# Optimization experiments

Measured on AMD Instinct MI355X. Metric: run time of the kernel, lower is better.

Reference implementation:

```python
import jax, jax.numpy as jnp
import numpy as np

B, L, C, H = 1024, 64, 1024, 16  # windows*batch, window area, dim, heads
D = C // H  # head_dim = 64
WIN = 64  # window_size[0]; window_size = (64, 1)


def _relative_position_index():
    coords = np.arange(WIN)
    idx = coords[:, None] - coords[None, :] + (WIN - 1)
    return jnp.asarray(idx, dtype=jnp.int32)  # [L, L]


def setup_inputs() -> dict:
    key = jax.random.key(0)
    ks = jax.random.split(key, 8)
    s = 0.02
    return {
        "hidden_states": jax.random.normal(ks[0], (B, L, C), dtype=jnp.float32),
        "Wq": jax.random.normal(ks[1], (C, C), dtype=jnp.float32) * s,
        "bq": jax.random.normal(ks[2], (C,), dtype=jnp.float32) * s,
        "Wk": jax.random.normal(ks[3], (C, C), dtype=jnp.float32) * s,
        "bk": jax.random.normal(ks[4], (C,), dtype=jnp.float32) * s,
        "Wv": jax.random.normal(ks[5], (C, C), dtype=jnp.float32) * s,
        "bv": jax.random.normal(ks[6], (C,), dtype=jnp.float32) * s,
        "bias_table": jax.random.normal(ks[7], (2 * WIN - 1, H), dtype=jnp.float32) * s,
        "rel_index": _relative_position_index(),
    }


def reference(hidden_states, Wq, bq, Wk, bk, Wv, bv, bias_table, rel_index):
    b, l, c = hidden_states.shape
    # QKV projections -> [b, H, l, D]
    q = (hidden_states @ Wq + bq).reshape(b, l, H, D).transpose(0, 2, 1, 3)
    k = (hidden_states @ Wk + bk).reshape(b, l, H, D).transpose(0, 2, 1, 3)
    v = (hidden_states @ Wv + bv).reshape(b, l, H, D).transpose(0, 2, 1, 3)
    scores = jnp.einsum("bhqd,bhkd->bhqk", q, k) / jnp.sqrt(jnp.float32(D))
    # relative position bias: gather [L, L, H] -> [1, H, L, L]
    rel_bias = bias_table[rel_index]  # [L, L, H]
    scores = scores + rel_bias.transpose(2, 0, 1)[None]
    probs = jax.nn.softmax(scores, axis=-1)  # dropout p=0.0 (eval)
    context = jnp.einsum("bhqk,bhkd->bhqd", probs, v)
    context = context.transpose(0, 2, 1, 3).reshape(b, l, c)
    return context
```

## Files before the change

kernel.cpp:

```cpp
#include <hip/hip_runtime.h>
#include <hip/hip_fp16.h>
#include <stdint.h>

typedef _Float16 f16;
typedef _Float16 f16x8 __attribute__((ext_vector_type(8)));
typedef float f32x4 __attribute__((ext_vector_type(4)));

__device__ __forceinline__ void gload_lds16(const void* g, void* l) {
    __builtin_amdgcn_global_load_lds(
        (const __attribute__((address_space(1))) void*)g,
        (__attribute__((address_space(3))) void*)l,
        16, 0, 0);
}

__global__ __launch_bounds__(256) void convert_x(const float* __restrict__ X,
                                                 f16* __restrict__ Xh) {
    size_t i = ((size_t)blockIdx.x * 256 + threadIdx.x) * 8;
    float4 a = *(const float4*)(X + i);
    float4 b = *(const float4*)(X + i + 4);
    f16x8 o;
    o[0] = (f16)a.x; o[1] = (f16)a.y; o[2] = (f16)a.z; o[3] = (f16)a.w;
    o[4] = (f16)b.x; o[5] = (f16)b.y; o[6] = (f16)b.z; o[7] = (f16)b.w;
    *(f16x8*)(Xh + i) = o;
}

__global__ __launch_bounds__(1024) void transpose_w(const float* __restrict__ Wq,
                                                    const float* __restrict__ Wk,
                                                    const float* __restrict__ Wv,
                                                    f16* __restrict__ Wt) {
    __shared__ float tile[32][33];
    const int w = blockIdx.z;
    const float* W = (w == 0) ? Wq : ((w == 1) ? Wk : Wv);
    const int n0 = blockIdx.x * 32, k0 = blockIdx.y * 32;
    const int tx = threadIdx.x, ty = threadIdx.y;
    tile[ty][tx] = W[(size_t)(k0 + ty) * 1024 + n0 + tx];
    __syncthreads();
    Wt[(size_t)(w * 1024 + n0 + ty) * 1024 + k0 + tx] = (f16)tile[tx][ty];
}

__global__ __launch_bounds__(256) void qkv_gemm(const f16* __restrict__ A,
                                                const f16* __restrict__ Bt,
                                                const float* __restrict__ bq,
                                                const float* __restrict__ bk,
                                                const float* __restrict__ bv,
                                                f16* __restrict__ Out) {
    __shared__ __align__(16) f16 sA[128][32];
    __shared__ __align__(16) f16 sB[128][32];

    const int tid  = threadIdx.x;
    const int wave = tid >> 6, lane = tid & 63;
    const int quad = lane >> 4, l16 = lane & 15;
    const int m0 = blockIdx.y * 128, n0 = blockIdx.x * 128;
    const int wm = (wave & 1) * 64, wn = (wave >> 1) * 64;

    const int srow = lane >> 2;
    const int scol = (lane & 3) * 8;
    const f16* gA = A  + (size_t)(m0 + wave * 32 + srow) * 1024 + scol;
    const f16* gB = Bt + (size_t)(n0 + wave * 32 + srow) * 1024 + scol;
    f16* lA = &sA[wave * 32][0];
    f16* lB = &sB[wave * 32][0];

    f32x4 acc[4][4] = {};

    for (int k0 = 0; k0 < 1024; k0 += 32) {
        gload_lds16(gA + k0,             lA);
        gload_lds16(gA + k0 + 16 * 1024, lA + 16 * 32);
        gload_lds16(gB + k0,             lB);
        gload_lds16(gB + k0 + 16 * 1024, lB + 16 * 32);
        __syncthreads();

        f16x8 af[4], bf[4];
#pragma unroll
        for (int t = 0; t < 4; ++t)
            af[t] = *(const f16x8*)&sA[wm + t * 16 + l16][quad * 8];
#pragma unroll
        for (int t = 0; t < 4; ++t)
            bf[t] = *(const f16x8*)&sB[wn + t * 16 + l16][quad * 8];

#pragma unroll
        for (int mt = 0; mt < 4; ++mt)
#pragma unroll
            for (int nt = 0; nt < 4; ++nt)
                acc[mt][nt] = __builtin_amdgcn_mfma_f32_16x16x32_f16(
                    af[mt], bf[nt], acc[mt][nt], 0, 0, 0);
        __syncthreads();
    }

    const int w_idx = n0 >> 10;
    const float* bias = (w_idx == 0) ? bq : ((w_idx == 1) ? bk : bv);
    f16* out = Out + (size_t)w_idx * (65536UL * 1024UL);
#pragma unroll
    for (int mt = 0; mt < 4; ++mt) {
#pragma unroll
        for (int r = 0; r < 4; ++r) {
            const int m = m0 + wm + mt * 16 + quad * 4 + r;
            const int b = m >> 6, l = m & 63;
#pragma unroll
            for (int nt = 0; nt < 4; ++nt) {
                const int n  = n0 + wn + nt * 16 + l16;
                const int nc = n & 1023;
                const int h = nc >> 6, d = nc & 63;
                const float v = acc[mt][nt][r] + bias[nc];
                out[(((size_t)b * 16 + h) * 64 + l) * 64 + d] = (f16)v;
            }
        }
    }
}

__global__ __launch_bounds__(256) void attn(const f16* __restrict__ QKV,
                                            const float* __restrict__ bias_table,
                                            float* __restrict__ outp) {
    __shared__ __align__(16) f16 sQ[64][72];
    __shared__ __align__(16) f16 sK[64][72];
    __shared__ __align__(16) f16 sVt[64][72];
    __shared__ float sS[64][66];
    __shared__ float sR[64];

    const int bh = blockIdx.x;
    const int h  = bh & 15;
    const int tid  = threadIdx.x;
    const int wave = tid >> 6, lane = tid & 63;
    const int quad = lane >> 4, l16 = lane & 15;

    const f16* Qg = QKV + (size_t)bh * 4096;
    const f16* Kg = Qg + 65536UL * 1024UL;
    const f16* Vg = Kg + 65536UL * 1024UL;

#pragma unroll
    for (int j = 0; j < 2; ++j) {
        const int idx = tid + j * 256;
        const int e = idx * 8;
        const int l = e >> 6, d = e & 63;
        *(f16x8*)&sQ[l][d] = *(const f16x8*)(Qg + e);
        *(f16x8*)&sK[l][d] = *(const f16x8*)(Kg + e);
        f16x8 v = *(const f16x8*)(Vg + e);
#pragma unroll
        for (int i = 0; i < 8; ++i) sVt[d + i][l] = v[i];
    }
    __syncthreads();

    {
        f32x4 acc[4] = {};
#pragma unroll
        for (int k0 = 0; k0 < 64; k0 += 32) {
            f16x8 a = *(const f16x8*)&sQ[wave * 16 + l16][k0 + quad * 8];
#pragma unroll
            for (int nt = 0; nt < 4; ++nt) {
                f16x8 b = *(const f16x8*)&sK[nt * 16 + l16][k0 + quad * 8];
                acc[nt] = __builtin_amdgcn_mfma_f32_16x16x32_f16(a, b, acc[nt], 0, 0, 0);
            }
        }
#pragma unroll
        for (int nt = 0; nt < 4; ++nt) {
            const int jcol = nt * 16 + l16;
#pragma unroll
            for (int r = 0; r < 4; ++r) {
                const int i = wave * 16 + quad * 4 + r;
                const float bias = bias_table[(i - jcol + 63) * 16 + h];
                sS[i][jcol] = acc[nt][r] * 0.125f + bias;
            }
        }
    }
    __syncthreads();

    if (tid < 64) {
        float mx = -1e30f;
#pragma unroll
        for (int j = 0; j < 64; ++j) mx = fmaxf(mx, sS[tid][j]);
        float sum = 0.f;
#pragma unroll
        for (int j = 0; j < 64; ++j) {
            const float e = __expf(sS[tid][j] - mx);
            sum += e;
            sQ[tid][j] = (f16)e;
        }
        sR[tid] = 1.0f / sum;
    }
    __syncthreads();

    {
        f32x4 acc[4] = {};
#pragma unroll
        for (int k0 = 0; k0 < 64; k0 += 32) {
            f16x8 a = *(const f16x8*)&sQ[wave * 16 + l16][k0 + quad * 8];
#pragma unroll
            for (int nt = 0; nt < 4; ++nt) {
                f16x8 b = *(const f16x8*)&sVt[nt * 16 + l16][k0 + quad * 8];
                acc[nt] = __builtin_amdgcn_mfma_f32_16x16x32_f16(a, b, acc[nt], 0, 0, 0);
            }
        }
        const int b = bh >> 4;
#pragma unroll
        for (int nt = 0; nt < 4; ++nt) {
            const int d = nt * 16 + l16;
#pragma unroll
            for (int r = 0; r < 4; ++r) {
                const int i = wave * 16 + quad * 4 + r;
                outp[((size_t)b * 64 + i) * 1024 + h * 64 + d] = acc[nt][r] * sR[i];
            }
        }
    }
}

extern "C" void kernel_launch(void* const* d_in, const int* in_sizes, int n_in,
                              void* d_out, int out_size, void* d_ws, size_t ws_size,
                              hipStream_t stream) {
    const float* X          = (const float*)d_in[0];
    const float* Wq         = (const float*)d_in[1];
    const float* bq         = (const float*)d_in[2];
    const float* Wk         = (const float*)d_in[3];
    const float* bk         = (const float*)d_in[4];
    const float* Wv         = (const float*)d_in[5];
    const float* bv         = (const float*)d_in[6];
    const float* bias_table = (const float*)d_in[7];
    float* out = (float*)d_out;

    f16* Xh  = (f16*)d_ws;
    f16* Wt  = Xh + 67108864UL;
    f16* QKV = Wt + 3145728UL;

    convert_x<<<32768, 256, 0, stream>>>(X, Xh);
    transpose_w<<<dim3(32, 32, 3), dim3(32, 32), 0, stream>>>(Wq, Wk, Wv, Wt);
    qkv_gemm<<<dim3(24, 512), 256, 0, stream>>>(Xh, Wt, bq, bk, bv, QKV);
    attn<<<16384, 256, 0, stream>>>(QKV, bias_table, out);
}
```

Measured before the change: 1.125 ms.

## Swizzle GEMM LDS, store V transposed, and keep attention softmax in registers

The QKV GEMM now XOR-swizzles the LDS column layout to cut bank conflicts on the fragment reads. Its epilogue writes V directly in [b,h,d,l] layout with vectorized f16x4 stores, so attention can load V^T with plain vector copies instead of scattered transposes. Attention keeps scores in MFMA accumulators and does the softmax with cross-lane shuffles. It also caches the per-head bias row in LDS, removing the fp32 score buffer and two block barriers. The trade-off is that correctness now relies on each wave writing and reading only its own rows of sQ, guarded by a waitcnt rather than a barrier.

```diff
diff --git a/kernel.cpp b/kernel.cpp
--- a/kernel.cpp
+++ b/kernel.cpp
@@ -3,6 +3,7 @@
 #include <stdint.h>
 
 typedef _Float16 f16;
+typedef _Float16 f16x4 __attribute__((ext_vector_type(4)));
 typedef _Float16 f16x8 __attribute__((ext_vector_type(8)));
 typedef float f32x4 __attribute__((ext_vector_type(4)));
 
@@ -54,11 +55,13 @@
     const int wm = (wave & 1) * 64, wn = (wave >> 1) * 64;
 
     const int srow = lane >> 2;
-    const int scol = (lane & 3) * 8;
+    const int scol = (((lane & 3) ^ ((lane >> 3) & 3))) * 8;
     const f16* gA = A  + (size_t)(m0 + wave * 32 + srow) * 1024 + scol;
     const f16* gB = Bt + (size_t)(n0 + wave * 32 + srow) * 1024 + scol;
     f16* lA = &sA[wave * 32][0];
     f16* lB = &sB[wave * 32][0];
+
+    const int fcol = (quad ^ ((l16 >> 1) & 3)) * 8;
 
     f32x4 acc[4][4] = {};
 
@@ -72,10 +75,10 @@
         f16x8 af[4], bf[4];
 #pragma unroll
         for (int t = 0; t < 4; ++t)
-            af[t] = *(const f16x8*)&sA[wm + t * 16 + l16][quad * 8];
+            af[t] = *(const f16x8*)&sA[wm + t * 16 + l16][fcol];
 #pragma unroll
         for (int t = 0; t < 4; ++t)
-            bf[t] = *(const f16x8*)&sB[wn + t * 16 + l16][quad * 8];
+            bf[t] = *(const f16x8*)&sB[wn + t * 16 + l16][fcol];
 
 #pragma unroll
         for (int mt = 0; mt < 4; ++mt)
@@ -89,19 +92,38 @@
     const int w_idx = n0 >> 10;
     const float* bias = (w_idx == 0) ? bq : ((w_idx == 1) ? bk : bv);
     f16* out = Out + (size_t)w_idx * (65536UL * 1024UL);
-#pragma unroll
-    for (int mt = 0; mt < 4; ++mt) {
-#pragma unroll
-        for (int r = 0; r < 4; ++r) {
-            const int m = m0 + wm + mt * 16 + quad * 4 + r;
-            const int b = m >> 6, l = m & 63;
+    if (w_idx < 2) {
+#pragma unroll
+        for (int mt = 0; mt < 4; ++mt) {
+#pragma unroll
+            for (int r = 0; r < 4; ++r) {
+                const int m = m0 + wm + mt * 16 + quad * 4 + r;
+                const int b = m >> 6, l = m & 63;
+#pragma unroll
+                for (int nt = 0; nt < 4; ++nt) {
+                    const int n  = n0 + wn + nt * 16 + l16;
+                    const int nc = n & 1023;
+                    const int h = nc >> 6, d = nc & 63;
+                    const float v = acc[mt][nt][r] + bias[nc];
+                    out[(((size_t)b * 16 + h) * 64 + l) * 64 + d] = (f16)v;
+                }
+            }
+        }
+    } else {
+#pragma unroll
+        for (int mt = 0; mt < 4; ++mt) {
+            const int mb = m0 + wm + mt * 16 + quad * 4;
+            const int b = mb >> 6, l = mb & 63;
 #pragma unroll
             for (int nt = 0; nt < 4; ++nt) {
                 const int n  = n0 + wn + nt * 16 + l16;
                 const int nc = n & 1023;
                 const int h = nc >> 6, d = nc & 63;
-                const float v = acc[mt][nt][r] + bias[nc];
-                out[(((size_t)b * 16 + h) * 64 + l) * 64 + d] = (f16)v;
+                f16x4 pv;
+#pragma unroll
+                for (int r = 0; r < 4; ++r)
+                    pv[r] = (f16)(acc[mt][nt][r] + bias[nc]);
+                *(f16x4*)&out[(((size_t)b * 16 + h) * 64 + d) * 64 + l] = pv;
             }
         }
     }
@@ -113,8 +135,7 @@
     __shared__ __align__(16) f16 sQ[64][72];
     __shared__ __align__(16) f16 sK[64][72];
     __shared__ __align__(16) f16 sVt[64][72];
-    __shared__ float sS[64][66];
-    __shared__ float sR[64];
+    __shared__ float sBias[128];
 
     const int bh = blockIdx.x;
     const int h  = bh & 15;
@@ -128,77 +149,76 @@
 
 #pragma unroll
     for (int j = 0; j < 2; ++j) {
-        const int idx = tid + j * 256;
-        const int e = idx * 8;
-        const int l = e >> 6, d = e & 63;
-        *(f16x8*)&sQ[l][d] = *(const f16x8*)(Qg + e);
-        *(f16x8*)&sK[l][d] = *(const f16x8*)(Kg + e);
-        f16x8 v = *(const f16x8*)(Vg + e);
-#pragma unroll
-        for (int i = 0; i < 8; ++i) sVt[d + i][l] = v[i];
-    }
+        const int e = (tid + j * 256) * 8;
+        const int r = e >> 6, c = e & 63;
+        *(f16x8*)&sQ[r][c]  = *(const f16x8*)(Qg + e);
+        *(f16x8*)&sK[r][c]  = *(const f16x8*)(Kg + e);
+        *(f16x8*)&sVt[r][c] = *(const f16x8*)(Vg + e);
+    }
+    if (tid < 127) sBias[tid] = bias_table[tid * 16 + h];
     __syncthreads();
 
-    {
-        f32x4 acc[4] = {};
-#pragma unroll
-        for (int k0 = 0; k0 < 64; k0 += 32) {
-            f16x8 a = *(const f16x8*)&sQ[wave * 16 + l16][k0 + quad * 8];
-#pragma unroll
-            for (int nt = 0; nt < 4; ++nt) {
-                f16x8 b = *(const f16x8*)&sK[nt * 16 + l16][k0 + quad * 8];
-                acc[nt] = __builtin_amdgcn_mfma_f32_16x16x32_f16(a, b, acc[nt], 0, 0, 0);
-            }
-        }
-#pragma unroll
-        for (int nt = 0; nt < 4; ++nt) {
-            const int jcol = nt * 16 + l16;
-#pragma unroll
-            for (int r = 0; r < 4; ++r) {
-                const int i = wave * 16 + quad * 4 + r;
-                const float bias = bias_table[(i - jcol + 63) * 16 + h];
-                sS[i][jcol] = acc[nt][r] * 0.125f + bias;
-            }
-        }
-    }
-    __syncthreads();
-
-    if (tid < 64) {
-        float mx = -1e30f;
-#pragma unroll
-        for (int j = 0; j < 64; ++j) mx = fmaxf(mx, sS[tid][j]);
+    f32x4 acc[4] = {};
+#pragma unroll
+    for (int k0 = 0; k0 < 64; k0 += 32) {
+        f16x8 a = *(const f16x8*)&sQ[wave * 16 + l16][k0 + quad * 8];
+#pragma unroll
+        for (int nt = 0; nt < 4; ++nt) {
+            f16x8 b = *(const f16x8*)&sK[nt * 16 + l16][k0 + quad * 8];
+            acc[nt] = __builtin_amdgcn_mfma_f32_16x16x32_f16(a, b, acc[nt], 0, 0, 0);
+        }
+    }
+
+    float rs[4];
+#pragma unroll
+    for (int r = 0; r < 4; ++r) {
+        const int i = wave * 16 + quad * 4 + r;
+#pragma unroll
+        for (int nt = 0; nt < 4; ++nt) {
+            const int j = nt * 16 + l16;
+            acc[nt][r] = acc[nt][r] * 0.125f + sBias[i - j + 63];
+        }
+        float mx = fmaxf(fmaxf(acc[0][r], acc[1][r]), fmaxf(acc[2][r], acc[3][r]));
+#pragma unroll
+        for (int m = 1; m < 16; m <<= 1) mx = fmaxf(mx, __shfl_xor(mx, m, 64));
         float sum = 0.f;
 #pragma unroll
-        for (int j = 0; j < 64; ++j) {
-            const float e = __expf(sS[tid][j] - mx);
-            sum += e;
-            sQ[tid][j] = (f16)e;
-        }
-        sR[tid] = 1.0f / sum;
-    }
-    __syncthreads();
-
-    {
-        f32x4 acc[4] = {};
-#pragma unroll
-        for (int k0 = 0; k0 < 64; k0 += 32) {
-            f16x8 a = *(const f16x8*)&sQ[wave * 16 + l16][k0 + quad * 8];
-#pragma unroll
-            for (int nt = 0; nt < 4; ++nt) {
-                f16x8 b = *(const f16x8*)&sVt[nt * 16 + l16][k0 + quad * 8];
-                acc[nt] = __builtin_amdgcn_mfma_f32_16x16x32_f16(a, b, acc[nt], 0, 0, 0);
-            }
-        }
-        const int b = bh >> 4;
-#pragma unroll
-        for (int nt = 0; nt < 4; ++nt) {
-            const int d = nt * 16 + l16;
-#pragma unroll
-            for (int r = 0; r < 4; ++r) {
-                const int i = wave * 16 + quad * 4 + r;
-                outp[((size_t)b * 64 + i) * 1024 + h * 64 + d] = acc[nt][r] * sR[i];
-            }
-        }
+        for (int nt = 0; nt < 4; ++nt) {
+            const float p = __expf(acc[nt][r] - mx);
+            acc[nt][r] = p;
+            sum += p;
+        }
+#pragma unroll
+        for (int m = 1; m < 16; m <<= 1) sum += __shfl_xor(sum, m, 64);
+        rs[r] = 1.0f / sum;
+    }
+
+#pragma unroll
+    for (int r = 0; r < 4; ++r)
+#pragma unroll
+        for (int nt = 0; nt < 4; ++nt)
+            sQ[wave * 16 + quad * 4 + r][nt * 16 + l16] = (f16)acc[nt][r];
+    __asm__ __volatile__("s_waitcnt lgkmcnt(0)" ::: "memory");
+
+    f32x4 o[4] = {};
+#pragma unroll
+    for (int k0 = 0; k0 < 64; k0 += 32) {
+        f16x8 a = *(const f16x8*)&sQ[wave * 16 + l16][k0 + quad * 8];
+#pragma unroll
+        for (int nt = 0; nt < 4; ++nt) {
+            f16x8 b = *(const f16x8*)&sVt[nt * 16 + l16][k0 + quad * 8];
+            o[nt] = __builtin_amdgcn_mfma_f32_16x16x32_f16(a, b, o[nt], 0, 0, 0);
+        }
+    }
+
+    const int b = bh >> 4;
+    float* op = outp + ((size_t)b * 64 + wave * 16) * 1024 + (size_t)h * 64;
+#pragma unroll
+    for (int nt = 0; nt < 4; ++nt) {
+        const int d = nt * 16 + l16;
+#pragma unroll
+        for (int r = 0; r < 4; ++r)
+            op[(quad * 4 + r) * 1024 + d] = o[nt][r] * rs[r];
     }
 }
 
```

Result: slower. 1.184 ms (+5.3%).
